# Optimization experiments

Hardware: AMD Instinct MI355X
Metric: run time of the kernel (lower is better)

Reference implementation:

```python
import jax, jax.numpy as jnp
import numpy as np

FILTER = [1.0, 3.0, 3.0, 1.0]  # filter_type
PAD = 1  # padding on each side


def _blur_kernel():
    k = jnp.asarray(FILTER, dtype=jnp.float32)
    kernel = jnp.outer(k, k)          # direction='vh' -> 4x4
    kernel = kernel / kernel.sum()
    return kernel


def setup_inputs() -> dict:
    key = jax.random.key(0)
    h = jax.random.normal(key, (8, 256, 64, 512), dtype=jnp.float32)
    return {"h": h}


def reference(h):
    # Pad: horizontal circular (ring=True), then vertical reflect.
    hp = jnp.pad(h, ((0, 0), (0, 0), (0, 0), (PAD, PAD)), mode='wrap')
    hp = jnp.pad(hp, ((0, 0), (0, 0), (PAD, PAD), (0, 0)), mode='reflect')
    C = h.shape[1]
    kernel = _blur_kernel()  # (4,4)
    # Depthwise conv: one 4x4 filter per channel (groups=C).
    w = jnp.broadcast_to(kernel[None, None], (C, 1, 4, 4))  # OIHW, I=1
    out = jax.lax.conv_general_dilated(
        hp, w,
        window_strides=(1, 1),
        padding='VALID',
        dimension_numbers=('NCHW', 'OIHW', 'NCHW'),
        feature_group_count=C,
    )
    return out  # (B, C, H-1, W-1) for 4x4 kernel with pad 1, stride 1
```

## Files before the change

### kernel.cpp

```cpp
#include <hip/hip_runtime.h>


constexpr int H_ = 64, W_ = 512;
constexpr int HO = 63, WO = 511;
constexpr int GROUPS = W_ / 4;

__device__ __forceinline__ float4 hblur_row(const float* __restrict__ row,
                                            int c0, int pcol, int bcol) {
    const float4 A  = *reinterpret_cast<const float4*>(row + c0);
    const float2 Bv = *reinterpret_cast<const float2*>(row + bcol);
    const float  p  = row[pcol];
    float4 r;
    r.x = fmaf(3.f, A.x + A.y, p   + A.z);
    r.y = fmaf(3.f, A.y + A.z, A.x + A.w);
    r.z = fmaf(3.f, A.z + A.w, A.y + Bv.x);
    r.w = fmaf(3.f, A.w + Bv.x, A.z + Bv.y);
    return r;
}

__global__ __launch_bounds__(256) void blur_kernel(const float* __restrict__ h,
                                                   float* __restrict__ out) {
    const int tid = blockIdx.x * blockDim.x + threadIdx.x;
    const int g   = tid & (GROUPS - 1);
    const int bc  = tid >> 7;

    const float* img = h   + (size_t)bc * (H_ * W_);
    float*       op  = out + (size_t)bc * (HO * WO);

    const int c0   = g * 4;
    const int pcol = (c0 - 1) & (W_ - 1);
    const int bcol = (c0 + 4) & (W_ - 1);

    float4 h0 = hblur_row(img + W_, c0, pcol, bcol);
    float4 h1 = hblur_row(img,      c0, pcol, bcol);
    float4 h2 = h0;

    const int nstore = (g == GROUPS - 1) ? 3 : 4;

    for (int oy = 0; oy < HO; ++oy) {
        const int p3 = oy + 3;
        const int r  = (p3 <= H_) ? (p3 - 1) : (H_ - 2);
        const float4 h3 = hblur_row(img + r * W_, c0, pcol, bcol);

        float o[4];
        o[0] = (h0.x + h3.x + 3.f * (h1.x + h2.x)) * (1.f / 64.f);
        o[1] = (h0.y + h3.y + 3.f * (h1.y + h2.y)) * (1.f / 64.f);
        o[2] = (h0.z + h3.z + 3.f * (h1.z + h2.z)) * (1.f / 64.f);
        o[3] = (h0.w + h3.w + 3.f * (h1.w + h2.w)) * (1.f / 64.f);

        float* dst = op + oy * WO + c0;
        #pragma unroll
        for (int k = 0; k < 4; ++k)
            if (k < nstore) dst[k] = o[k];

        h0 = h1; h1 = h2; h2 = h3;
    }
}

extern "C" void kernel_launch(void* const* d_in, const int* in_sizes, int n_in,
                              void* d_out, int out_size, void* d_ws, size_t ws_size,
                              hipStream_t stream) {
    const float* h = (const float*)d_in[0];
    float* out = (float*)d_out;

    const int total = 2048 * GROUPS;
    const int block = 256;
    const int grid  = total / block;
    blur_kernel<<<grid, block, 0, stream>>>(h, out);
}
```

Baseline: 474.6 us.

## Split each image's rows into four chunks and use nontemporal stores

Each thread now handles a 16-row vertical chunk instead of all 63 output rows, which quadruples the thread count so more waves are in flight to hide memory latency. Each chunk recomputes three halo rows of horizontal blur, adding about 19% more reads, which should mostly hit cache. The loop is unrolled by 4 and output stores use nontemporal hints to avoid polluting cache. The output is 511 wide, so stores are unaligned scalar writes either way.

```diff
diff --git a/kernel.cpp b/kernel.cpp
--- a/kernel.cpp
+++ b/kernel.cpp
@@ -4,6 +4,14 @@
 constexpr int H_ = 64, W_ = 512;
 constexpr int HO = 63, WO = 511;
 constexpr int GROUPS = W_ / 4;
+constexpr int NCHUNK = 4, CHUNK = 16;
+
+__device__ __forceinline__ int rowmap(int p) {
+    int r = p - 1;
+    if (p == 0)  r = 1;
+    if (p > H_)  r = H_ - 2;
+    return r;
+}
 
 __device__ __forceinline__ float4 hblur_row(const float* __restrict__ row,
                                             int c0, int pcol, int bcol) {
@@ -20,9 +28,10 @@
 
 __global__ __launch_bounds__(256) void blur_kernel(const float* __restrict__ h,
                                                    float* __restrict__ out) {
-    const int tid = blockIdx.x * blockDim.x + threadIdx.x;
-    const int g   = tid & (GROUPS - 1);
-    const int bc  = tid >> 7;
+    const int tid   = blockIdx.x * blockDim.x + threadIdx.x;
+    const int g     = tid & (GROUPS - 1);
+    const int chunk = (tid >> 7) & (NCHUNK - 1);
+    const int bc    = tid >> 9;
 
     const float* img = h   + (size_t)bc * (H_ * W_);
     float*       op  = out + (size_t)bc * (HO * WO);
@@ -31,16 +40,19 @@
     const int pcol = (c0 - 1) & (W_ - 1);
     const int bcol = (c0 + 4) & (W_ - 1);
 
-    float4 h0 = hblur_row(img + W_, c0, pcol, bcol);
-    float4 h1 = hblur_row(img,      c0, pcol, bcol);
-    float4 h2 = h0;
+    const int oy0 = chunk * CHUNK;
+    const int R   = min(CHUNK, HO - oy0);
+
+    float4 h0 = hblur_row(img + rowmap(oy0)     * W_, c0, pcol, bcol);
+    float4 h1 = hblur_row(img + rowmap(oy0 + 1) * W_, c0, pcol, bcol);
+    float4 h2 = hblur_row(img + rowmap(oy0 + 2) * W_, c0, pcol, bcol);
 
     const int nstore = (g == GROUPS - 1) ? 3 : 4;
 
-    for (int oy = 0; oy < HO; ++oy) {
-        const int p3 = oy + 3;
-        const int r  = (p3 <= H_) ? (p3 - 1) : (H_ - 2);
-        const float4 h3 = hblur_row(img + r * W_, c0, pcol, bcol);
+    #pragma unroll 4
+    for (int j = 0; j < R; ++j) {
+        const int p3 = oy0 + j + 3;
+        const float4 h3 = hblur_row(img + rowmap(p3) * W_, c0, pcol, bcol);
 
         float o[4];
         o[0] = (h0.x + h3.x + 3.f * (h1.x + h2.x)) * (1.f / 64.f);
@@ -48,10 +60,10 @@
         o[2] = (h0.z + h3.z + 3.f * (h1.z + h2.z)) * (1.f / 64.f);
         o[3] = (h0.w + h3.w + 3.f * (h1.w + h2.w)) * (1.f / 64.f);
 
-        float* dst = op + oy * WO + c0;
+        float* dst = op + (size_t)(oy0 + j) * WO + c0;
         #pragma unroll
         for (int k = 0; k < 4; ++k)
-            if (k < nstore) dst[k] = o[k];
+            if (k < nstore) __builtin_nontemporal_store(o[k], dst + k);
 
         h0 = h1; h1 = h2; h2 = h3;
     }
@@ -63,7 +75,7 @@
     const float* h = (const float*)d_in[0];
     float* out = (float*)d_out;
 
-    const int total = 2048 * GROUPS;
+    const int total = 2048 * NCHUNK * GROUPS;
     const int block = 256;
     const int grid  = total / block;
     blur_kernel<<<grid, block, 0, stream>>>(h, out);
```

New measurement: 498.0 us. +4.9%, slower.
